# Kernel optimization log

Hardware: AMD Instinct MI355X
Metric: run time of the kernel (lower is better)

## Reference

```python
import jax, jax.numpy as jnp
import numpy as np

BLOCK_SIZE = 512


def setup_inputs() -> dict:
    key = jax.random.key(0)
    k1, k2, k3 = jax.random.split(key, 3)
    N, D_IN, NUM_BLOCKS = 8192, 2048, 8
    x = jax.random.normal(k1, (N, D_IN), dtype=jnp.float32)
    # Rademacher +/-1 signs per block
    s_hash = jnp.sign(jax.random.normal(k2, (NUM_BLOCKS, D_IN), dtype=jnp.float32))
    s_hash = jnp.where(s_hash == 0, 1.0, s_hash)
    # hash bucket index in [0, BLOCK_SIZE) per block, per input dim
    i_hash = jax.random.randint(k3, (NUM_BLOCKS, D_IN), 0, BLOCK_SIZE, dtype=jnp.int32)
    return {"x": x, "s_hash": s_hash, "i_hash": i_hash}


def reference(x, s_hash, i_hash):
    # x: [N, d_in]; s_hash: [B, d_in] (+/-1); i_hash: [B, d_in] in [0, block_size)
    N = x.shape[0]
    B = s_hash.shape[0]

    def one_block(s, ih):
        y = x * s  # [N, d_in] sign flip
        # scatter-add columns into block_size buckets (duplicates accumulate)
        return jnp.zeros((N, BLOCK_SIZE), x.dtype).at[:, ih].add(y)

    out = jax.vmap(one_block)(s_hash, i_hash)      # [B, N, block_size]
    out = jnp.moveaxis(out, 0, 1).reshape(N, B * BLOCK_SIZE)  # [N, d_features]
    return out / np.sqrt(B).astype(np.float32)
```

## Files before the change

### kernel.cpp

```cpp
#include <hip/hip_runtime.h>
#include <cstddef>

#define NUM_BLOCKS 8
#define BLK 512
#define D_IN 2048
#define NROWS 8192
#define NBUCKETS (NUM_BLOCKS * BLK)
#define CAP 32
#define ROWS_PER_WG 8
#define THREADS 512
#define SENT 4096

typedef float    v4f __attribute__((ext_vector_type(4)));
typedef unsigned v4u __attribute__((ext_vector_type(4)));

__global__ __launch_bounds__(256) void cs_build_index(
    const int* __restrict__ i_hash, const float* __restrict__ s_hash,
    int* __restrict__ nchunks, int* __restrict__ entries,
    unsigned short* __restrict__ entries16)
{
    const int gid  = blockIdx.x * blockDim.x + threadIdx.x;
    const int wave = gid >> 6;
    const int lane = threadIdx.x & 63;
    if (wave >= NBUCKETS) return;
    const int b = wave >> 9;
    const int k = wave & (BLK - 1);
    const int*   ih = i_hash + b * D_IN;
    const float* sr = s_hash + b * D_IN;
    int* erow = entries + wave * CAP;
    unsigned short* e16 = entries16 + wave * 8;
    int cnt = 0;
    for (int d0 = 0; d0 < D_IN; d0 += 64) {
        const int d = d0 + lane;
        const bool m = (ih[d] == k);
        const unsigned long long mask = __ballot(m);
        if (m) {
            const int pos = cnt + __popcll(mask & ((1ull << lane) - 1ull));
            const int ent = (d << 1) | ((sr[d] < 0.0f) ? 1 : 0);
            if (pos < CAP) erow[pos] = ent;
            if (pos < 8)   e16[pos]  = (unsigned short)ent;
        }
        cnt += (int)__popcll(mask);
    }
    if (cnt > CAP) cnt = CAP;
    int nch = (cnt + 3) >> 2;
    if (nch == 0) nch = 1;
    if (lane >= cnt) {
        if (lane < 8)       e16[lane]  = (unsigned short)SENT;
        if (lane < nch * 4) erow[lane] = SENT;
    }
    if (lane == 0) nchunks[wave] = nch;
}

__global__ __launch_bounds__(THREADS, 4) void cs_gather(
    const float* __restrict__ x, const int* __restrict__ nchunks,
    const int* __restrict__ entries, const v4u* __restrict__ entries16,
    float* __restrict__ out)
{
    __shared__ v4u xs4[D_IN + 1];
    const int tid  = threadIdx.x;
    const int row0 = blockIdx.x * ROWS_PER_WG;

    v4u e8[8];
    int nch[8];
#pragma unroll
    for (int g = 0; g < 2; ++g)
#pragma unroll
        for (int q = 0; q < 4; ++q) {
            const int j = 4 * (tid + 512 * g) + q;
            e8[g * 4 + q]  = entries16[j];
            nch[g * 4 + q] = nchunks[j];
        }

    if (tid == 0) xs4[D_IN] = (v4u){0u, 0u, 0u, 0u};

    const size_t b0 = (size_t)row0 * D_IN;
#pragma unroll
    for (int i = 0; i < 4; ++i) {
        const int d = tid + i * THREADS;
        unsigned r[8];
#pragma unroll
        for (int rr = 0; rr < 8; ++rr) {
            const unsigned u = __float_as_uint(x[b0 + (size_t)rr * D_IN + d]);
            r[rr] = (u + 0x7fffu + ((u >> 16) & 1u)) >> 16;
        }
        v4u w;
        w.x = r[0] | (r[1] << 16);
        w.y = r[2] | (r[3] << 16);
        w.z = r[4] | (r[5] << 16);
        w.w = r[6] | (r[7] << 16);
        xs4[d] = w;
    }
    __syncthreads();

    const float scale = 0.35355339059327373f;
#define ASF __uint_as_float

#define PE(e, A)                                                          \
    do {                                                                  \
        const unsigned ue = (unsigned)(e);                                \
        const unsigned sm = (ue & 1u) ? 0x80008000u : 0u;                 \
        const v4u w = xs4[ue >> 1];                                       \
        const unsigned w0 = w.x ^ sm, w1 = w.y ^ sm;                      \
        const unsigned w2 = w.z ^ sm, w3 = w.w ^ sm;                      \
        A[0] += ASF(w0 << 16); A[1] += ASF(w0 & 0xffff0000u);             \
        A[2] += ASF(w1 << 16); A[3] += ASF(w1 & 0xffff0000u);             \
        A[4] += ASF(w2 << 16); A[5] += ASF(w2 & 0xffff0000u);             \
        A[6] += ASF(w3 << 16); A[7] += ASF(w3 & 0xffff0000u);             \
    } while (0)

#pragma unroll
    for (int g = 0; g < 2; ++g) {
        const int col4 = tid + 512 * g;
        float acc[4][8];
#pragma unroll
        for (int q = 0; q < 4; ++q)
#pragma unroll
            for (int rr = 0; rr < 8; ++rr) acc[q][rr] = 0.0f;

#pragma unroll
        for (int q = 0; q < 4; ++q) {
            const v4u ew = e8[g * 4 + q];
            PE(ew.x & 0xffffu, acc[q]); PE(ew.x >> 16, acc[q]);
            PE(ew.y & 0xffffu, acc[q]); PE(ew.y >> 16, acc[q]);
            PE(ew.z & 0xffffu, acc[q]); PE(ew.z >> 16, acc[q]);
            PE(ew.w & 0xffffu, acc[q]);
            PE(ew.w >> 16, acc[q]);
            const int n = nch[g * 4 + q];
            if (n > 2) {
                const int j = 4 * col4 + q;
                const int4* __restrict__ ep = (const int4*)(entries + j * CAP);
#pragma unroll 1
                for (int c = 2; c < n; ++c) {
                    const int4 cc = ep[c];
                    PE(cc.x, acc[q]); PE(cc.y, acc[q]);
                    PE(cc.z, acc[q]); PE(cc.w, acc[q]);
                }
            }
        }
#pragma unroll
        for (int rr = 0; rr < 8; ++rr) {
            v4f v = { acc[0][rr] * scale, acc[1][rr] * scale,
                      acc[2][rr] * scale, acc[3][rr] * scale };
            __builtin_nontemporal_store(
                v, (v4f*)(out + (size_t)(row0 + rr) * NBUCKETS + 4 * col4));
        }
    }
#undef PE
#undef ASF
}

extern "C" void kernel_launch(void* const* d_in, const int* in_sizes, int n_in,
                              void* d_out, int out_size, void* d_ws, size_t ws_size,
                              hipStream_t stream)
{
    const float* x      = (const float*)d_in[0];
    const float* s_hash = (const float*)d_in[1];
    const int*   i_hash = (const int*)d_in[2];
    float* out = (float*)d_out;

    int* nchunks = (int*)d_ws;
    int* entries = nchunks + NBUCKETS;
    unsigned short* entries16 = (unsigned short*)(entries + NBUCKETS * CAP);

    cs_build_index<<<(NBUCKETS * 64) / 256, 256, 0, stream>>>(
        i_hash, s_hash, nchunks, entries, entries16);
    cs_gather<<<NROWS / ROWS_PER_WG, THREADS, 0, stream>>>(
        x, nchunks, entries, (const v4u*)entries16, out);
}
```

Before: 56.15 us.

## Split gather into two 4-row halves, prefetching second half during first compute

```diff
diff --git a/kernel.cpp b/kernel.cpp
--- a/kernel.cpp
+++ b/kernel.cpp
@@ -52,12 +52,17 @@
     if (lane == 0) nchunks[wave] = nch;
 }
 
-__global__ __launch_bounds__(THREADS, 4) void cs_gather(
+static __device__ __forceinline__ unsigned bfr(float f) {
+    const unsigned u = __float_as_uint(f);
+    return (u + 0x7fffu + ((u >> 16) & 1u)) >> 16;
+}
+
+__global__ __launch_bounds__(THREADS) void cs_gather(
     const float* __restrict__ x, const int* __restrict__ nchunks,
     const int* __restrict__ entries, const v4u* __restrict__ entries16,
     float* __restrict__ out)
 {
-    __shared__ v4u xs4[D_IN + 1];
+    __shared__ uint2 xs2[2][D_IN + 8];
     const int tid  = threadIdx.x;
     const int row0 = blockIdx.x * ROWS_PER_WG;
 
@@ -72,81 +77,106 @@
             nch[g * 4 + q] = nchunks[j];
         }
 
-    if (tid == 0) xs4[D_IN] = (v4u){0u, 0u, 0u, 0u};
+    if (tid < 2) xs2[tid][D_IN] = make_uint2(0u, 0u);
 
     const size_t b0 = (size_t)row0 * D_IN;
+    const size_t b1 = b0 + (size_t)4 * D_IN;
+
 #pragma unroll
     for (int i = 0; i < 4; ++i) {
         const int d = tid + i * THREADS;
-        unsigned r[8];
-#pragma unroll
-        for (int rr = 0; rr < 8; ++rr) {
-            const unsigned u = __float_as_uint(x[b0 + (size_t)rr * D_IN + d]);
-            r[rr] = (u + 0x7fffu + ((u >> 16) & 1u)) >> 16;
-        }
-        v4u w;
-        w.x = r[0] | (r[1] << 16);
-        w.y = r[2] | (r[3] << 16);
-        w.z = r[4] | (r[5] << 16);
-        w.w = r[6] | (r[7] << 16);
-        xs4[d] = w;
-    }
-    __syncthreads();
+        uint2 w;
+        w.x = bfr(x[b0 + d]) | (bfr(x[b0 + D_IN + d]) << 16);
+        w.y = bfr(x[b0 + 2 * D_IN + d]) | (bfr(x[b0 + 3 * D_IN + d]) << 16);
+        xs2[0][d] = w;
+    }
+    float f1[4][4];
+#pragma unroll
+    for (int i = 0; i < 4; ++i) {
+        const int d = tid + i * THREADS;
+#pragma unroll
+        for (int rr = 0; rr < 4; ++rr)
+            f1[i][rr] = x[b1 + (size_t)rr * D_IN + d];
+    }
+    asm volatile("s_waitcnt lgkmcnt(0)" ::: "memory");
+    __builtin_amdgcn_s_barrier();
 
     const float scale = 0.35355339059327373f;
 #define ASF __uint_as_float
 
-#define PE(e, A)                                                          \
+#define PE4(e, A, XB)                                                     \
     do {                                                                  \
         const unsigned ue = (unsigned)(e);                                \
         const unsigned sm = (ue & 1u) ? 0x80008000u : 0u;                 \
-        const v4u w = xs4[ue >> 1];                                       \
+        const uint2 w = (XB)[ue >> 1];                                    \
         const unsigned w0 = w.x ^ sm, w1 = w.y ^ sm;                      \
-        const unsigned w2 = w.z ^ sm, w3 = w.w ^ sm;                      \
         A[0] += ASF(w0 << 16); A[1] += ASF(w0 & 0xffff0000u);             \
         A[2] += ASF(w1 << 16); A[3] += ASF(w1 & 0xffff0000u);             \
-        A[4] += ASF(w2 << 16); A[5] += ASF(w2 & 0xffff0000u);             \
-        A[6] += ASF(w3 << 16); A[7] += ASF(w3 & 0xffff0000u);             \
     } while (0)
 
-#pragma unroll
-    for (int g = 0; g < 2; ++g) {
-        const int col4 = tid + 512 * g;
-        float acc[4][8];
-#pragma unroll
-        for (int q = 0; q < 4; ++q)
-#pragma unroll
-            for (int rr = 0; rr < 8; ++rr) acc[q][rr] = 0.0f;
-
-#pragma unroll
-        for (int q = 0; q < 4; ++q) {
-            const v4u ew = e8[g * 4 + q];
-            PE(ew.x & 0xffffu, acc[q]); PE(ew.x >> 16, acc[q]);
-            PE(ew.y & 0xffffu, acc[q]); PE(ew.y >> 16, acc[q]);
-            PE(ew.z & 0xffffu, acc[q]); PE(ew.z >> 16, acc[q]);
-            PE(ew.w & 0xffffu, acc[q]);
-            PE(ew.w >> 16, acc[q]);
-            const int n = nch[g * 4 + q];
-            if (n > 2) {
-                const int j = 4 * col4 + q;
-                const int4* __restrict__ ep = (const int4*)(entries + j * CAP);
-#pragma unroll 1
-                for (int c = 2; c < n; ++c) {
-                    const int4 cc = ep[c];
-                    PE(cc.x, acc[q]); PE(cc.y, acc[q]);
-                    PE(cc.z, acc[q]); PE(cc.w, acc[q]);
-                }
-            }
-        }
-#pragma unroll
-        for (int rr = 0; rr < 8; ++rr) {
-            v4f v = { acc[0][rr] * scale, acc[1][rr] * scale,
-                      acc[2][rr] * scale, acc[3][rr] * scale };
-            __builtin_nontemporal_store(
-                v, (v4f*)(out + (size_t)(row0 + rr) * NBUCKETS + 4 * col4));
-        }
-    }
-#undef PE
+#define COMPUTE_HALF(h)                                                   \
+    do {                                                                  \
+        const uint2* __restrict__ XB = &xs2[h][0];                        \
+        _Pragma("unroll")                                                 \
+        for (int g = 0; g < 2; ++g) {                                     \
+            const int col4 = tid + 512 * g;                               \
+            float acc[4][4];                                              \
+            _Pragma("unroll")                                             \
+            for (int q = 0; q < 4; ++q)                                   \
+                _Pragma("unroll")                                         \
+                for (int rr = 0; rr < 4; ++rr) acc[q][rr] = 0.0f;         \
+            _Pragma("unroll")                                             \
+            for (int q = 0; q < 4; ++q) {                                 \
+                const v4u ew = e8[g * 4 + q];                             \
+                PE4(ew.x & 0xffffu, acc[q], XB);                          \
+                PE4(ew.x >> 16,     acc[q], XB);                          \
+                PE4(ew.y & 0xffffu, acc[q], XB);                          \
+                PE4(ew.y >> 16,     acc[q], XB);                          \
+                PE4(ew.z & 0xffffu, acc[q], XB);                          \
+                PE4(ew.z >> 16,     acc[q], XB);                          \
+                PE4(ew.w & 0xffffu, acc[q], XB);                          \
+                PE4(ew.w >> 16,     acc[q], XB);                          \
+                const int n = nch[g * 4 + q];                             \
+                if (n > 2) {                                              \
+                    const int j = 4 * col4 + q;                           \
+                    const int4* __restrict__ ep =                         \
+                        (const int4*)(entries + j * CAP);                 \
+                    _Pragma("unroll 1")                                   \
+                    for (int c = 2; c < n; ++c) {                         \
+                        const int4 cc = ep[c];                            \
+                        PE4(cc.x, acc[q], XB); PE4(cc.y, acc[q], XB);     \
+                        PE4(cc.z, acc[q], XB); PE4(cc.w, acc[q], XB);     \
+                    }                                                     \
+                }                                                         \
+            }                                                             \
+            _Pragma("unroll")                                             \
+            for (int rr = 0; rr < 4; ++rr) {                              \
+                v4f v = { acc[0][rr] * scale, acc[1][rr] * scale,         \
+                          acc[2][rr] * scale, acc[3][rr] * scale };       \
+                __builtin_nontemporal_store(                              \
+                    v, (v4f*)(out + (size_t)(row0 + 4 * (h) + rr) *       \
+                              NBUCKETS + 4 * col4));                      \
+            }                                                             \
+        }                                                                 \
+    } while (0)
+
+    COMPUTE_HALF(0);
+
+#pragma unroll
+    for (int i = 0; i < 4; ++i) {
+        const int d = tid + i * THREADS;
+        uint2 w;
+        w.x = bfr(f1[i][0]) | (bfr(f1[i][1]) << 16);
+        w.y = bfr(f1[i][2]) | (bfr(f1[i][3]) << 16);
+        xs2[1][d] = w;
+    }
+    asm volatile("s_waitcnt lgkmcnt(0)" ::: "memory");
+    __builtin_amdgcn_s_barrier();
+
+    COMPUTE_HALF(1);
+
+#undef COMPUTE_HALF
+#undef PE4
 #undef ASF
 }
 
```

Result: slower. 70.02 us (+24.7%).
